# Kernel tuning notes

Hardware: AMD Instinct MI355X
Metric: run time of the kernel (lower is better)

The kernel has to match this reference:

```python
import jax, jax.numpy as jnp
import numpy as np

B, S, D_IN = 4, 2048, 1024
H, D_HEAD = 16, 64  # per-head output dim d_output=64


def setup_inputs() -> dict:
    key = jax.random.key(0)
    ks = jax.random.split(key, 9)
    s_in = 1.0 / np.sqrt(D_IN)
    s_o = 1.0 / np.sqrt(H * D_HEAD)
    return {
        "x": jax.random.normal(ks[0], (B, S, D_IN), dtype=jnp.float32),
        "Wq": jax.random.uniform(ks[1], (H, D_IN, D_HEAD), jnp.float32, -s_in, s_in),
        "bq": jax.random.uniform(ks[2], (H, D_HEAD), jnp.float32, -s_in, s_in),
        "Wk": jax.random.uniform(ks[3], (H, D_IN, D_HEAD), jnp.float32, -s_in, s_in),
        "bk": jax.random.uniform(ks[4], (H, D_HEAD), jnp.float32, -s_in, s_in),
        "Wv": jax.random.uniform(ks[5], (H, D_IN, D_HEAD), jnp.float32, -s_in, s_in),
        "bv": jax.random.uniform(ks[6], (H, D_HEAD), jnp.float32, -s_in, s_in),
        "Wo": jax.random.uniform(ks[7], (H * D_HEAD, D_HEAD), jnp.float32, -s_o, s_o),
        "bo": jax.random.uniform(ks[8], (D_HEAD,), jnp.float32, -s_o, s_o),
    }


def reference(x, Wq, bq, Wk, bk, Wv, bv, Wo, bo):
    # per-head projections: [B,H,S,Dh]
    q = jnp.einsum("bsd,hde->bhse", x, Wq) + bq[None, :, None, :]
    k = jnp.einsum("bsd,hde->bhse", x, Wk) + bk[None, :, None, :]
    v = jnp.einsum("bsd,hde->bhse", x, Wv) + bv[None, :, None, :]
    scale = 1.0 / np.sqrt(D_HEAD)
    scores = jnp.einsum("bhqe,bhke->bhqk", q, k) * scale  # [B,H,S,S]
    seq_len = x.shape[1]
    causal = jnp.tril(jnp.ones((seq_len, seq_len), dtype=bool))
    scores = jnp.where(causal[None, None], scores, -jnp.inf)
    attn = jax.nn.softmax(scores, axis=-1)  # dropout=0 -> identity
    out = jnp.einsum("bhqk,bhke->bhqe", attn, v)  # [B,H,S,Dh]
    # concat heads along feature dim (head order matches torch cat)
    out = out.transpose(0, 2, 1, 3).reshape(x.shape[0], seq_len, H * D_HEAD)
    return out @ Wo + bo
```

## Files before the change

kernel.cpp:

```cpp
#include <hip/hip_runtime.h>

typedef unsigned short u16;
typedef unsigned int u32;
typedef __attribute__((ext_vector_type(8))) short s16x8;
typedef __attribute__((ext_vector_type(4))) float f32x4;

#define MFMA(a,b,c) __builtin_amdgcn_mfma_f32_16x16x32_bf16((a),(b),(c),0,0,0)
#define QSCALE 0.18033688011112042f

__device__ __forceinline__ u16 bfc(float f){
  union { float f; unsigned int u; } c; c.f = f;
  return (u16)((c.u + 0x7fffu + ((c.u >> 16) & 1u)) >> 16);
}
__device__ __forceinline__ u32 pkbf(float lo, float hi){
  union { float f; u32 u; } a, b; a.f = lo; b.f = hi;
  return __builtin_amdgcn_perm(b.u + 0x8000u, a.u + 0x8000u, 0x07060302u);
}
__device__ __forceinline__ float fexp2(float x){ return __builtin_amdgcn_exp2f(x); }
__device__ __forceinline__ f32x4 zero4(){ f32x4 z; z[0]=0.f; z[1]=0.f; z[2]=0.f; z[3]=0.f; return z; }

__device__ __forceinline__ void gload_lds16(const u16* g, u16* l){
  __builtin_amdgcn_global_load_lds((const __attribute__((address_space(1))) unsigned int*)g,
                                   (__attribute__((address_space(3))) unsigned int*)l, 16, 0, 0);
}

__global__ __launch_bounds__(256) void k_cvt(const float* __restrict__ x, u16* __restrict__ xb){
  int i = (blockIdx.x * 256 + threadIdx.x) * 4;
  float4 v = *(const float4*)(x + i);
  *(uint2*)(xb + i) = make_uint2(pkbf(v.x, v.y), pkbf(v.z, v.w));
}

__global__ __launch_bounds__(256) void k_twp(const float* __restrict__ Wq, const float* __restrict__ Wk,
    const float* __restrict__ Wv, const float* __restrict__ Wo,
    u16* __restrict__ wt, u16* __restrict__ wot){
  __shared__ float t[64][65];
  int y = blockIdx.y, k0 = blockIdx.x * 64, tid = threadIdx.x;
  const float* src; u16* dst;
  if (y < 16)      { src = Wq + (size_t)y * 65536;        dst = wt + (size_t)y * 65536; }
  else if (y < 32) { src = Wk + (size_t)(y-16) * 65536;   dst = wt + (size_t)y * 65536; }
  else if (y < 48) { src = Wv + (size_t)(y-32) * 65536;   dst = wt + (size_t)y * 65536; }
  else             { src = Wo;                            dst = wot; }
  const float* s = src + (size_t)k0 * 64;
  int kl = tid >> 2, nc = (tid & 3) * 16;
  #pragma unroll
  for (int j = 0; j < 4; j++){
    float4 v = *(const float4*)(s + kl * 64 + nc + j * 4);
    t[kl][nc + j*4 + 0] = v.x; t[kl][nc + j*4 + 1] = v.y;
    t[kl][nc + j*4 + 2] = v.z; t[kl][nc + j*4 + 3] = v.w;
  }
  __syncthreads();
  int n = tid >> 2, kc = (tid & 3) * 16;
  u16 o[16];
  #pragma unroll
  for (int j = 0; j < 16; j++) o[j] = bfc(t[kc + j][n]);
  u16* d = dst + (size_t)n * 1024 + k0 + kc;
  *(uint4*)(d)     = *(uint4*)&o[0];
  *(uint4*)(d + 8) = *(uint4*)&o[8];
}

__global__ __launch_bounds__(256) void k_qkv(const u16* __restrict__ xb, const u16* __restrict__ wt,
    const float* __restrict__ bq, const float* __restrict__ bk, const float* __restrict__ bv,
    u16* __restrict__ Qo, u16* __restrict__ Ko, u16* __restrict__ VT){
  __shared__ u16 As[128][64];
  __shared__ u16 Bs[128][64];
  int tid = threadIdx.x, wave = tid >> 6, lane = tid & 63;
  int l16 = lane & 15, g = lane >> 4;
  int row0 = blockIdx.x * 128, col0 = blockIdx.y * 128;
  int wm = (wave & 1) * 64, wn = (wave >> 1) * 64;
  f32x4 acc[4][4];
  #pragma unroll
  for (int mt = 0; mt < 4; mt++)
    #pragma unroll
    for (int nt = 0; nt < 4; nt++) acc[mt][nt] = zero4();
  int srow = (lane >> 3);
  int scol = ((lane & 7) ^ srow) * 8;
  for (int k0 = 0; k0 < 1024; k0 += 64){
    __syncthreads();
    #pragma unroll
    for (int p = 0; p < 4; p++){
      int r = wave * 32 + p * 8 + srow;
      gload_lds16(xb + (size_t)(row0 + r) * 1024 + k0 + scol, &As[wave * 32 + p * 8][0]);
      gload_lds16(wt + (size_t)(col0 + r) * 1024 + k0 + scol, &Bs[wave * 32 + p * 8][0]);
    }
    __syncthreads();
    #pragma unroll
    for (int c = 0; c < 2; c++){
      s16x8 af[4], bf[4];
      #pragma unroll
      for (int mt = 0; mt < 4; mt++)
        af[mt] = *(const s16x8*)&As[wm + mt*16 + l16][((c*4 + g) ^ (l16 & 7)) * 8];
      #pragma unroll
      for (int nt = 0; nt < 4; nt++)
        bf[nt] = *(const s16x8*)&Bs[wn + nt*16 + l16][((c*4 + g) ^ (l16 & 7)) * 8];
      #pragma unroll
      for (int mt = 0; mt < 4; mt++)
        #pragma unroll
        for (int nt = 0; nt < 4; nt++) acc[mt][nt] = MFMA(af[mt], bf[nt], acc[mt][nt]);
    }
  }
  #pragma unroll
  for (int nt = 0; nt < 4; nt++){
    int n = col0 + wn + nt * 16 + l16;
    int wi = n >> 10, hh = (n >> 6) & 15, dh = n & 63;
    const float* bptr = (wi == 0) ? bq : (wi == 1) ? bk : bv;
    float bval = bptr[hh * 64 + dh];
    #pragma unroll
    for (int mt = 0; mt < 4; mt++){
      int m0 = row0 + wm + mt * 16 + g * 4;
      int bb = m0 >> 11, ss = m0 & 2047;
      if (wi == 2){
        u32 p0 = pkbf(acc[mt][nt][0] + bval, acc[mt][nt][1] + bval);
        u32 p1 = pkbf(acc[mt][nt][2] + bval, acc[mt][nt][3] + bval);
        *(uint2*)&VT[(((size_t)bb * 16 + hh) * 64 + dh) * 2048 + ss] = make_uint2(p0, p1);
      } else {
        u16* dst = (wi == 0) ? Qo : Ko;
        float scl = (wi == 0) ? QSCALE : 1.0f;
        #pragma unroll
        for (int i = 0; i < 4; i++)
          dst[(((size_t)bb * 16 + hh) * 2048 + ss + i) * 64 + dh] = bfc((acc[mt][nt][i] + bval) * scl);
      }
    }
  }
}

__global__ __launch_bounds__(256, 3) void k_attn(const u16* __restrict__ Q, const u16* __restrict__ Kg,
    const u16* __restrict__ VT, u16* __restrict__ O){
  __shared__ u16 smem[18432];
  u16* Ks = smem;
  u16* Vt = smem + 4608;
  u16* Ps = smem + 9216;
  int hbi = blockIdx.x;
  int qt = 15 - (int)blockIdx.y;
  int b = hbi >> 4, h = hbi & 15;
  int tid = threadIdx.x, wave = tid >> 6, lane = tid & 63;
  int l16 = lane & 15, g = lane >> 4;
  size_t hb = (size_t)hbi * 2048 * 64;
  const u16* kbase = Kg + hb;
  const u16* vbase = VT + hb;
  int sr = tid >> 3, scc = (tid & 7) * 8;
  u16* PsW = Ps + wave * (32 * 72);
  int q0 = qt * 128 + wave * 32;
  s16x8 bq[2][2];
  #pragma unroll
  for (int j = 0; j < 2; j++)
    #pragma unroll
    for (int c = 0; c < 2; c++)
      bq[j][c] = *(const s16x8*)(Q + hb + (size_t)(q0 + j*16 + l16) * 64 + c*32 + g*8);
  f32x4 accO[4][2];
  #pragma unroll
  for (int mt = 0; mt < 4; mt++)
    #pragma unroll
    for (int j = 0; j < 2; j++) accO[mt][j] = zero4();
  float rs0 = 0.f, rs1 = 0.f;
  int nkt = 2 * qt + 2;
  uint4 ka0, ka1, va0, va1;
  ka0 = *(const uint4*)(kbase + (size_t)(sr)      * 64 + scc);
  ka1 = *(const uint4*)(kbase + (size_t)(sr + 32) * 64 + scc);
  va0 = *(const uint4*)(vbase + (size_t)(sr)      * 2048 + scc);
  va1 = *(const uint4*)(vbase + (size_t)(sr + 32) * 2048 + scc);
  *(uint4*)&Ks[sr * 72 + scc] = ka0; *(uint4*)&Ks[(sr + 32) * 72 + scc] = ka1;
  *(uint4*)&Vt[sr * 72 + scc] = va0; *(uint4*)&Vt[(sr + 32) * 72 + scc] = va1;
  __syncthreads();
  for (int kt = 0; kt < nkt; kt++){
    if (kt + 1 < nkt){
      int kb2 = (kt + 1) * 64;
      ka0 = *(const uint4*)(kbase + (size_t)(kb2 + sr)      * 64 + scc);
      ka1 = *(const uint4*)(kbase + (size_t)(kb2 + sr + 32) * 64 + scc);
      va0 = *(const uint4*)(vbase + (size_t)(sr)      * 2048 + kb2 + scc);
      va1 = *(const uint4*)(vbase + (size_t)(sr + 32) * 2048 + kb2 + scc);
    }
    int ks0 = kt * 64;
    if (ks0 <= q0 + 31){
      #pragma unroll
      for (int kb = 0; kb < 4; kb++){
        s16x8 ak0 = *(const s16x8*)&Ks[(kb*16 + l16) * 72 + g*8];
        s16x8 ak1 = *(const s16x8*)&Ks[(kb*16 + l16) * 72 + 32 + g*8];
        #pragma unroll
        for (int j = 0; j < 2; j++){
          f32x4 s = zero4();
          s = MFMA(ak0, bq[j][0], s);
          s = MFMA(ak1, bq[j][1], s);
          if (ks0 + kb*16 + 15 > q0 + j*16){
            int qrow = q0 + j*16 + l16;
            #pragma unroll
            for (int r = 0; r < 4; r++)
              if (ks0 + kb*16 + g*4 + r > qrow) s[r] = -1e30f;
          }
          float p0 = fexp2(s[0]), p1 = fexp2(s[1]), p2 = fexp2(s[2]), p3 = fexp2(s[3]);
          if (j == 0) rs0 += (p0 + p1) + (p2 + p3);
          else        rs1 += (p0 + p1) + (p2 + p3);
          *(uint2*)&PsW[(j*16 + l16) * 72 + kb*16 + g*4] = make_uint2(pkbf(p0, p1), pkbf(p2, p3));
        }
      }
      s16x8 av[4][2];
      #pragma unroll
      for (int mt = 0; mt < 4; mt++)
        #pragma unroll
        for (int kc = 0; kc < 2; kc++)
          av[mt][kc] = *(const s16x8*)&Vt[(mt*16 + l16) * 72 + kc*32 + g*8];
      #pragma unroll
      for (int j = 0; j < 2; j++){
        s16x8 bp0 = *(const s16x8*)&PsW[(j*16 + l16) * 72 + g*8];
        s16x8 bp1 = *(const s16x8*)&PsW[(j*16 + l16) * 72 + 32 + g*8];
        #pragma unroll
        for (int mt = 0; mt < 4; mt++){
          accO[mt][j] = MFMA(av[mt][0], bp0, accO[mt][j]);
          accO[mt][j] = MFMA(av[mt][1], bp1, accO[mt][j]);
        }
      }
    }
    if (kt + 1 < nkt){
      __syncthreads();
      *(uint4*)&Ks[sr * 72 + scc] = ka0; *(uint4*)&Ks[(sr + 32) * 72 + scc] = ka1;
      *(uint4*)&Vt[sr * 72 + scc] = va0; *(uint4*)&Vt[(sr + 32) * 72 + scc] = va1;
      __syncthreads();
    }
  }
  float rinv[2];
  #pragma unroll
  for (int j = 0; j < 2; j++){
    float l = (j == 0) ? rs0 : rs1;
    l += __shfl_xor(l, 16);
    l += __shfl_xor(l, 32);
    rinv[j] = 1.0f / l;
  }
  #pragma unroll
  for (int mt = 0; mt < 4; mt++)
    #pragma unroll
    for (int j = 0; j < 2; j++){
      float o0 = accO[mt][j][0] * rinv[j];
      float o1 = accO[mt][j][1] * rinv[j];
      float o2 = accO[mt][j][2] * rinv[j];
      float o3 = accO[mt][j][3] * rinv[j];
      *(uint2*)&O[((size_t)b * 2048 + q0 + j*16 + l16) * 1024 + h*64 + mt*16 + g*4] =
          make_uint2(pkbf(o0, o1), pkbf(o2, o3));
    }
}

__global__ __launch_bounds__(256) void k_oproj(const u16* __restrict__ Ob, const u16* __restrict__ wot,
    const float* __restrict__ bo, float* __restrict__ out){
  __shared__ u16 As[64][72];
  __shared__ u16 Bs[64][72];
  int rb = blockIdx.x, kc = blockIdx.y;
  int tid = threadIdx.x, wave = tid >> 6, lane = tid & 63;
  int l16 = lane & 15, g = lane >> 4;
  int wr = (wave & 1) * 32, wc = (wave >> 1) * 32;
  int row0 = rb * 64;
  f32x4 acc[2][2];
  acc[0][0]=zero4(); acc[0][1]=zero4(); acc[1][0]=zero4(); acc[1][1]=zero4();
  int r0s = tid >> 3, cc0 = (tid & 7) * 8, r1s = r0s + 32;
  for (int k0 = kc * 256; k0 < kc * 256 + 256; k0 += 64){
    __syncthreads();
    *(uint4*)&As[r0s][cc0] = *(const uint4*)(Ob + (size_t)(row0 + r0s) * 1024 + k0 + cc0);
    *(uint4*)&As[r1s][cc0] = *(const uint4*)(Ob + (size_t)(row0 + r1s) * 1024 + k0 + cc0);
    *(uint4*)&Bs[r0s][cc0] = *(const uint4*)(wot + (size_t)r0s * 1024 + k0 + cc0);
    *(uint4*)&Bs[r1s][cc0] = *(const uint4*)(wot + (size_t)r1s * 1024 + k0 + cc0);
    __syncthreads();
    #pragma unroll
    for (int c = 0; c < 2; c++){
      int kcc = c * 32;
      s16x8 a0 = *(const s16x8*)&As[wr      + l16][kcc + g * 8];
      s16x8 a1 = *(const s16x8*)&As[wr + 16 + l16][kcc + g * 8];
      s16x8 b0 = *(const s16x8*)&Bs[wc      + l16][kcc + g * 8];
      s16x8 b1 = *(const s16x8*)&Bs[wc + 16 + l16][kcc + g * 8];
      acc[0][0] = MFMA(a0, b0, acc[0][0]);
      acc[0][1] = MFMA(a0, b1, acc[0][1]);
      acc[1][0] = MFMA(a1, b0, acc[1][0]);
      acc[1][1] = MFMA(a1, b1, acc[1][1]);
    }
  }
  #pragma unroll
  for (int rt = 0; rt < 2; rt++){
    #pragma unroll
    for (int ct = 0; ct < 2; ct++){
      int col = wc + ct * 16 + l16;
      float bval = (kc == 0) ? bo[col] : 0.f;
      #pragma unroll
      for (int i = 0; i < 4; i++){
        int row = row0 + wr + rt * 16 + g * 4 + i;
        atomicAdd(&out[(size_t)row * 64 + col], acc[rt][ct][i] + bval);
      }
    }
  }
}

extern "C" void kernel_launch(void* const* d_in, const int* in_sizes, int n_in,
                              void* d_out, int out_size, void* d_ws, size_t ws_size,
                              hipStream_t stream){
  const float* x  = (const float*)d_in[0];
  const float* Wq = (const float*)d_in[1];
  const float* bq = (const float*)d_in[2];
  const float* Wk = (const float*)d_in[3];
  const float* bk = (const float*)d_in[4];
  const float* Wv = (const float*)d_in[5];
  const float* bv = (const float*)d_in[6];
  const float* Wo = (const float*)d_in[7];
  const float* bo = (const float*)d_in[8];

  u16* xb  = (u16*)d_ws;
  u16* wt  = xb  + 8388608;
  u16* wot = wt  + 3145728;
  u16* Qb  = wot + 65536;
  u16* Kb  = Qb  + 8388608;
  u16* VTb = Kb  + 8388608;
  u16* Ob  = xb;
  float* out = (float*)d_out;

  hipMemsetAsync(d_out, 0, (size_t)out_size * sizeof(float), stream);
  k_cvt<<<8192, 256, 0, stream>>>(x, xb);
  k_twp<<<dim3(16, 49), 256, 0, stream>>>(Wq, Wk, Wv, Wo, wt, wot);
  k_qkv<<<dim3(64, 24), 256, 0, stream>>>(xb, wt, bq, bk, bv, Qb, Kb, VTb);
  k_attn<<<dim3(64, 16), 256, 0, stream>>>(Qb, Kb, VTb, Ob);
  k_oproj<<<dim3(128, 4), 256, 0, stream>>>(Ob, wot, bo, out);
}
```

Baseline: 234.1 us.

## Restructure QKV GEMM into 256x256 tiles with a four-stage LDS load pipeline

The QKV projection GEMM moves from 128x128 tiles with 4 waves to 256x256 tiles with 8 waves. Four waves load A and four load B into a 4-slot ring buffer that uses a new swizzled layout, and loads run three stages ahead under explicit vmcnt waits and raw barriers. MFMA sections are wrapped in setprio. The aim is more data reuse per tile and overlap of global-to-LDS loads with MFMA work, at the cost of 128 KB of LDS per block, higher register pressure, and only 384 blocks in the grid.

```diff
diff --git a/kernel.cpp b/kernel.cpp
--- a/kernel.cpp
+++ b/kernel.cpp
@@ -7,6 +7,9 @@
 
 #define MFMA(a,b,c) __builtin_amdgcn_mfma_f32_16x16x32_bf16((a),(b),(c),0,0,0)
 #define QSCALE 0.18033688011112042f
+
+#define BAR() do { asm volatile("" ::: "memory"); __builtin_amdgcn_s_barrier(); asm volatile("" ::: "memory"); } while(0)
+#define WAITV(n) asm volatile("s_waitcnt vmcnt(" #n ")" ::: "memory")
 
 __device__ __forceinline__ u16 bfc(float f){
   union { float f; unsigned int u; } c; c.f = f;
@@ -58,55 +61,92 @@
   *(uint4*)(d + 8) = *(uint4*)&o[8];
 }
 
-__global__ __launch_bounds__(256) void k_qkv(const u16* __restrict__ xb, const u16* __restrict__ wt,
+__global__ __launch_bounds__(512, 2) void k_qkv(const u16* __restrict__ xb, const u16* __restrict__ wt,
     const float* __restrict__ bq, const float* __restrict__ bk, const float* __restrict__ bv,
     u16* __restrict__ Qo, u16* __restrict__ Ko, u16* __restrict__ VT){
-  __shared__ u16 As[128][64];
-  __shared__ u16 Bs[128][64];
-  int tid = threadIdx.x, wave = tid >> 6, lane = tid & 63;
+  __shared__ u16 lds[65536];
+  u16* Ab = lds;
+  u16* Bb = lds + 32768;
+  int tid = threadIdx.x, w = tid >> 6, lane = tid & 63;
   int l16 = lane & 15, g = lane >> 4;
-  int row0 = blockIdx.x * 128, col0 = blockIdx.y * 128;
-  int wm = (wave & 1) * 64, wn = (wave >> 1) * 64;
-  f32x4 acc[4][4];
-  #pragma unroll
-  for (int mt = 0; mt < 4; mt++)
+  int wm = w >> 2, wn = w & 3;
+  int row0 = blockIdx.x * 256, col0 = blockIdx.y * 256;
+  f32x4 acc[8][4];
+  #pragma unroll
+  for (int mt = 0; mt < 8; mt++)
     #pragma unroll
     for (int nt = 0; nt < 4; nt++) acc[mt][nt] = zero4();
-  int srow = (lane >> 3);
-  int scol = ((lane & 7) ^ srow) * 8;
-  for (int k0 = 0; k0 < 1024; k0 += 64){
-    __syncthreads();
-    #pragma unroll
-    for (int p = 0; p < 4; p++){
-      int r = wave * 32 + p * 8 + srow;
-      gload_lds16(xb + (size_t)(row0 + r) * 1024 + k0 + scol, &As[wave * 32 + p * 8][0]);
-      gload_lds16(wt + (size_t)(col0 + r) * 1024 + k0 + scol, &Bs[wave * 32 + p * 8][0]);
-    }
-    __syncthreads();
-    #pragma unroll
-    for (int c = 0; c < 2; c++){
-      s16x8 af[4], bf[4];
-      #pragma unroll
-      for (int mt = 0; mt < 4; mt++)
-        af[mt] = *(const s16x8*)&As[wm + mt*16 + l16][((c*4 + g) ^ (l16 & 7)) * 8];
+
+  bool isB = (w >= 4);
+  int wseg = (w & 3) * 4;
+  const u16* gsrc = isB ? wt : xb;
+  int gbase0 = isB ? col0 : row0;
+  const u16* gp[4];
+  #pragma unroll
+  for (int j = 0; j < 4; j++){
+    int sg = wseg + j;
+    int r = sg * 8 + (lane >> 3);
+    int pc = lane & 7;
+    int lc = pc ^ (r & 7);
+    int m = 2 * r + (lc >> 2);
+    int kk = (lc & 3) * 8;
+    gp[j] = gsrc + (size_t)(gbase0 + m) * 1024 + kk;
+  }
+  u16* lring = isB ? Bb : Ab;
+
+  auto stage = [&](int s3){
+    u16* lslot = lring + (s3 & 3) * 8192;
+    int ko = s3 * 32;
+    #pragma unroll
+    for (int j = 0; j < 4; j++)
+      gload_lds16(gp[j] + ko, lslot + (wseg + j) * 512);
+  };
+
+  auto phase = [&](int s){
+    const u16* Asl = Ab + (s & 3) * 8192;
+    const u16* Bsl = Bb + (s & 3) * 8192;
+    s16x8 af[8], bf[4];
+    #pragma unroll
+    for (int nt = 0; nt < 4; nt++){
+      int nr = wn * 64 + nt * 16 + l16;
+      int r = nr >> 1, pc = (((nr & 1) << 2) | g) ^ (r & 7);
+      bf[nt] = *(const s16x8*)&Bsl[r * 64 + pc * 8];
+    }
+    #pragma unroll
+    for (int mt = 0; mt < 8; mt++){
+      int mr = wm * 128 + mt * 16 + l16;
+      int r = mr >> 1, pc = (((mr & 1) << 2) | g) ^ (r & 7);
+      af[mt] = *(const s16x8*)&Asl[r * 64 + pc * 8];
+    }
+    __builtin_amdgcn_s_setprio(1);
+    #pragma unroll
+    for (int mt = 0; mt < 8; mt++)
       #pragma unroll
       for (int nt = 0; nt < 4; nt++)
-        bf[nt] = *(const s16x8*)&Bs[wn + nt*16 + l16][((c*4 + g) ^ (l16 & 7)) * 8];
-      #pragma unroll
-      for (int mt = 0; mt < 4; mt++)
-        #pragma unroll
-        for (int nt = 0; nt < 4; nt++) acc[mt][nt] = MFMA(af[mt], bf[nt], acc[mt][nt]);
-    }
-  }
+        acc[mt][nt] = MFMA(af[mt], bf[nt], acc[mt][nt]);
+    __builtin_amdgcn_s_setprio(0);
+  };
+
+  stage(0); stage(1); stage(2);
+  for (int s = 0; s < 29; ++s){
+    WAITV(8);
+    BAR();
+    stage(s + 3);
+    phase(s);
+  }
+  WAITV(8); BAR(); phase(29);
+  WAITV(4); BAR(); phase(30);
+  WAITV(0); BAR(); phase(31);
+
   #pragma unroll
   for (int nt = 0; nt < 4; nt++){
-    int n = col0 + wn + nt * 16 + l16;
+    int n = col0 + wn * 64 + nt * 16 + l16;
     int wi = n >> 10, hh = (n >> 6) & 15, dh = n & 63;
     const float* bptr = (wi == 0) ? bq : (wi == 1) ? bk : bv;
     float bval = bptr[hh * 64 + dh];
     #pragma unroll
-    for (int mt = 0; mt < 4; mt++){
-      int m0 = row0 + wm + mt * 16 + g * 4;
+    for (int mt = 0; mt < 8; mt++){
+      int m0 = row0 + wm * 128 + mt * 16 + g * 4;
       int bb = m0 >> 11, ss = m0 & 2047;
       if (wi == 2){
         u32 p0 = pkbf(acc[mt][nt][0] + bval, acc[mt][nt][1] + bval);
@@ -309,7 +349,7 @@
   hipMemsetAsync(d_out, 0, (size_t)out_size * sizeof(float), stream);
   k_cvt<<<8192, 256, 0, stream>>>(x, xb);
   k_twp<<<dim3(16, 49), 256, 0, stream>>>(Wq, Wk, Wv, Wo, wt, wot);
-  k_qkv<<<dim3(64, 24), 256, 0, stream>>>(xb, wt, bq, bk, bv, Qb, Kb, VTb);
+  k_qkv<<<dim3(32, 12), 512, 0, stream>>>(xb, wt, bq, bk, bv, Qb, Kb, VTb);
   k_attn<<<dim3(64, 16), 256, 0, stream>>>(Qb, Kb, VTb, Ob);
   k_oproj<<<dim3(128, 4), 256, 0, stream>>>(Ob, wot, bo, out);
 }
```

Result: slower. 238.8 us (+2.0%).

## Double-buffer QKV projection GEMM K-loop with async LDS prefetch

Applied to the files above, without the earlier changes.

Restructures the QKV projection GEMM main loop to use a 32-wide K step with two LDS buffers. The next tile is prefetched via global_load_lds while MFMAs run on the current one, with one barrier per step instead of two. It adds s_setprio around the MFMA block and a new XOR swizzle for the narrower rows. The trade-off is twice as many loop iterations with less MFMA work per barrier.

```diff
diff --git a/kernel.cpp b/kernel.cpp
--- a/kernel.cpp
+++ b/kernel.cpp
@@ -7,6 +7,9 @@
 
 #define MFMA(a,b,c) __builtin_amdgcn_mfma_f32_16x16x32_bf16((a),(b),(c),0,0,0)
 #define QSCALE 0.18033688011112042f
+
+#define BAR() do { asm volatile("" ::: "memory"); __builtin_amdgcn_s_barrier(); asm volatile("" ::: "memory"); } while(0)
+#define WAITV0() asm volatile("s_waitcnt vmcnt(0)" ::: "memory")
 
 __device__ __forceinline__ u16 bfc(float f){
   union { float f; unsigned int u; } c; c.f = f;
@@ -61,43 +64,69 @@
 __global__ __launch_bounds__(256) void k_qkv(const u16* __restrict__ xb, const u16* __restrict__ wt,
     const float* __restrict__ bq, const float* __restrict__ bk, const float* __restrict__ bv,
     u16* __restrict__ Qo, u16* __restrict__ Ko, u16* __restrict__ VT){
-  __shared__ u16 As[128][64];
-  __shared__ u16 Bs[128][64];
-  int tid = threadIdx.x, wave = tid >> 6, lane = tid & 63;
+  __shared__ u16 lds[16384];
+  int tid = threadIdx.x, w = tid >> 6, lane = tid & 63;
   int l16 = lane & 15, g = lane >> 4;
   int row0 = blockIdx.x * 128, col0 = blockIdx.y * 128;
-  int wm = (wave & 1) * 64, wn = (wave >> 1) * 64;
+  int wm = (w & 1) * 64, wn = (w >> 1) * 64;
   f32x4 acc[4][4];
   #pragma unroll
   for (int mt = 0; mt < 4; mt++)
     #pragma unroll
     for (int nt = 0; nt < 4; nt++) acc[mt][nt] = zero4();
-  int srow = (lane >> 3);
-  int scol = ((lane & 7) ^ srow) * 8;
-  for (int k0 = 0; k0 < 1024; k0 += 64){
-    __syncthreads();
-    #pragma unroll
-    for (int p = 0; p < 4; p++){
-      int r = wave * 32 + p * 8 + srow;
-      gload_lds16(xb + (size_t)(row0 + r) * 1024 + k0 + scol, &As[wave * 32 + p * 8][0]);
-      gload_lds16(wt + (size_t)(col0 + r) * 1024 + k0 + scol, &Bs[wave * 32 + p * 8][0]);
-    }
-    __syncthreads();
-    #pragma unroll
-    for (int c = 0; c < 2; c++){
-      s16x8 af[4], bf[4];
-      #pragma unroll
-      for (int mt = 0; mt < 4; mt++)
-        af[mt] = *(const s16x8*)&As[wm + mt*16 + l16][((c*4 + g) ^ (l16 & 7)) * 8];
-      #pragma unroll
-      for (int nt = 0; nt < 4; nt++)
-        bf[nt] = *(const s16x8*)&Bs[wn + nt*16 + l16][((c*4 + g) ^ (l16 & 7)) * 8];
-      #pragma unroll
-      for (int mt = 0; mt < 4; mt++)
-        #pragma unroll
-        for (int nt = 0; nt < 4; nt++) acc[mt][nt] = MFMA(af[mt], bf[nt], acc[mt][nt]);
-    }
-  }
+
+  int trow = tid >> 2;
+  int lc = (tid & 3) ^ ((tid >> 3) & 3);
+  const u16* gpa = xb + (size_t)(row0 + trow) * 1024 + lc * 8;
+  const u16* gpb = wt + (size_t)(col0 + trow) * 1024 + lc * 8;
+  u16* lA0 = &lds[w * 512];
+  u16* lA1 = &lds[2048 + w * 512];
+  u16* lB0 = &lds[8192 + w * 512];
+  u16* lB1 = &lds[8192 + 2048 + w * 512];
+
+  int afo[4], bfo[4];
+  #pragma unroll
+  for (int mt = 0; mt < 4; mt++){
+    int r = wm + mt * 16 + l16;
+    afo[mt] = r * 32 + ((g ^ ((r >> 1) & 3)) * 8);
+  }
+  #pragma unroll
+  for (int nt = 0; nt < 4; nt++){
+    int r = wn + nt * 16 + l16;
+    bfo[nt] = 8192 + r * 32 + ((g ^ ((r >> 1) & 3)) * 8);
+  }
+
+  gload_lds16(gpa,              lA0);
+  gload_lds16(gpa + 64 * 1024,  lA1);
+  gload_lds16(gpb,              lB0);
+  gload_lds16(gpb + 64 * 1024,  lB1);
+  WAITV0(); BAR();
+
+  #pragma unroll 2
+  for (int s = 0; s < 32; ++s){
+    if (s < 31){
+      int ko = (s + 1) * 32;
+      int dsel = ((s + 1) & 1) * 4096;
+      gload_lds16(gpa + ko,             lA0 + dsel);
+      gload_lds16(gpa + ko + 64 * 1024, lA1 + dsel);
+      gload_lds16(gpb + ko,             lB0 + dsel);
+      gload_lds16(gpb + ko + 64 * 1024, lB1 + dsel);
+    }
+    int sel = (s & 1) * 4096;
+    s16x8 af[4], bf[4];
+    #pragma unroll
+    for (int mt = 0; mt < 4; mt++) af[mt] = *(const s16x8*)&lds[sel + afo[mt]];
+    #pragma unroll
+    for (int nt = 0; nt < 4; nt++) bf[nt] = *(const s16x8*)&lds[sel + bfo[nt]];
+    __builtin_amdgcn_s_setprio(1);
+    #pragma unroll
+    for (int mt = 0; mt < 4; mt++)
+      #pragma unroll
+      for (int nt = 0; nt < 4; nt++) acc[mt][nt] = MFMA(af[mt], bf[nt], acc[mt][nt]);
+    __builtin_amdgcn_s_setprio(0);
+    WAITV0(); BAR();
+  }
+
   #pragma unroll
   for (int nt = 0; nt < 4; nt++){
     int n = col0 + wn + nt * 16 + l16;
```

New measurement: 232.2 us. No clear change (-0.8%).

## Restructure QKV GEMM with 256x128 tiles, 3-stage LDS pipeline and tile swizzle

Applied to the files above, without the earlier changes.

Rewrites the QKV projection GEMM to use 512-thread blocks on 256x128 output tiles with K-steps of 32. Global-to-LDS loads are triple-buffered with explicit vmcnt waits and raw barriers, so copies overlap the MFMA work. The block index is swizzled for L2 locality, and MFMA issue priority is raised while the MFMAs run. This targets load latency and sync stalls in the GEMM, at the cost of more LDS per block and hand-managed waitcnt ordering that can break correctness if the counts are wrong.

```diff
diff --git a/kernel.cpp b/kernel.cpp
--- a/kernel.cpp
+++ b/kernel.cpp
@@ -7,6 +7,9 @@
 
 #define MFMA(a,b,c) __builtin_amdgcn_mfma_f32_16x16x32_bf16((a),(b),(c),0,0,0)
 #define QSCALE 0.18033688011112042f
+
+#define BAR() do { asm volatile("" ::: "memory"); __builtin_amdgcn_s_barrier(); asm volatile("" ::: "memory"); } while(0)
+#define WAITV(n) asm volatile("s_waitcnt vmcnt(" #n ")" ::: "memory")
 
 __device__ __forceinline__ u16 bfc(float f){
   union { float f; unsigned int u; } c; c.f = f;
@@ -58,55 +61,75 @@
   *(uint4*)(d + 8) = *(uint4*)&o[8];
 }
 
-__global__ __launch_bounds__(256) void k_qkv(const u16* __restrict__ xb, const u16* __restrict__ wt,
+__global__ __launch_bounds__(512, 2) void k_qkv(const u16* __restrict__ xb, const u16* __restrict__ wt,
     const float* __restrict__ bq, const float* __restrict__ bk, const float* __restrict__ bv,
     u16* __restrict__ Qo, u16* __restrict__ Ko, u16* __restrict__ VT){
-  __shared__ u16 As[128][64];
-  __shared__ u16 Bs[128][64];
-  int tid = threadIdx.x, wave = tid >> 6, lane = tid & 63;
+  __shared__ u16 lds[36864];
+  int tid = threadIdx.x, w = tid >> 6, lane = tid & 63;
   int l16 = lane & 15, g = lane >> 4;
-  int row0 = blockIdx.x * 128, col0 = blockIdx.y * 128;
-  int wm = (wave & 1) * 64, wn = (wave >> 1) * 64;
+  int lin = (int)blockIdx.y * 32 + (int)blockIdx.x;
+  int swz = (lin & 7) * 96 + (lin >> 3);
+  int row0 = (swz & 31) * 256, col0 = (swz >> 5) * 128;
+  int wm = w >> 1, wn = w & 1;
   f32x4 acc[4][4];
   #pragma unroll
   for (int mt = 0; mt < 4; mt++)
     #pragma unroll
     for (int nt = 0; nt < 4; nt++) acc[mt][nt] = zero4();
-  int srow = (lane >> 3);
-  int scol = ((lane & 7) ^ srow) * 8;
-  for (int k0 = 0; k0 < 1024; k0 += 64){
-    __syncthreads();
-    #pragma unroll
-    for (int p = 0; p < 4; p++){
-      int r = wave * 32 + p * 8 + srow;
-      gload_lds16(xb + (size_t)(row0 + r) * 1024 + k0 + scol, &As[wave * 32 + p * 8][0]);
-      gload_lds16(wt + (size_t)(col0 + r) * 1024 + k0 + scol, &Bs[wave * 32 + p * 8][0]);
-    }
-    __syncthreads();
-    #pragma unroll
-    for (int c = 0; c < 2; c++){
-      s16x8 af[4], bf[4];
-      #pragma unroll
-      for (int mt = 0; mt < 4; mt++)
-        af[mt] = *(const s16x8*)&As[wm + mt*16 + l16][((c*4 + g) ^ (l16 & 7)) * 8];
-      #pragma unroll
-      for (int nt = 0; nt < 4; nt++)
-        bf[nt] = *(const s16x8*)&Bs[wn + nt*16 + l16][((c*4 + g) ^ (l16 & 7)) * 8];
-      #pragma unroll
-      for (int mt = 0; mt < 4; mt++)
-        #pragma unroll
-        for (int nt = 0; nt < 4; nt++) acc[mt][nt] = MFMA(af[mt], bf[nt], acc[mt][nt]);
-    }
+
+  int trow = tid >> 2;
+  int lc = (tid & 3) ^ ((tid >> 3) & 3);
+  const u16* gpa0 = xb + (size_t)(row0 + trow) * 1024 + lc * 8;
+  const u16* gpa1 = xb + (size_t)(row0 + 128 + trow) * 1024 + lc * 8;
+  const u16* gpb  = wt + (size_t)(col0 + trow) * 1024 + lc * 8;
+
+  int afo[4], bfo[4];
+  #pragma unroll
+  for (int mt = 0; mt < 4; mt++){
+    int r = wm * 64 + mt * 16 + l16;
+    afo[mt] = r * 32 + ((g ^ ((r >> 1) & 3)) * 8);
   }
   #pragma unroll
   for (int nt = 0; nt < 4; nt++){
-    int n = col0 + wn + nt * 16 + l16;
+    int r = wn * 64 + nt * 16 + l16;
+    bfo[nt] = 8192 + r * 32 + ((g ^ ((r >> 1) & 3)) * 8);
+  }
+
+#define STAGE(T2, SB) do { int ko_ = (T2) * 32; \
+    gload_lds16(gpa0 + ko_, &lds[(SB) + w * 512]); \
+    gload_lds16(gpa1 + ko_, &lds[(SB) + 4096 + w * 512]); \
+    gload_lds16(gpb  + ko_, &lds[(SB) + 8192 + w * 512]); } while(0)
+
+#define COMPUTE(SB) do { s16x8 af[4], bf[4]; \
+    _Pragma("unroll") for (int mt = 0; mt < 4; mt++) af[mt] = *(const s16x8*)&lds[(SB) + afo[mt]]; \
+    _Pragma("unroll") for (int nt = 0; nt < 4; nt++) bf[nt] = *(const s16x8*)&lds[(SB) + bfo[nt]]; \
+    __builtin_amdgcn_s_setprio(1); \
+    _Pragma("unroll") for (int mt = 0; mt < 4; mt++) \
+      _Pragma("unroll") for (int nt = 0; nt < 4; nt++) acc[mt][nt] = MFMA(af[mt], bf[nt], acc[mt][nt]); \
+    __builtin_amdgcn_s_setprio(0); } while(0)
+
+  STAGE(0, 0); STAGE(1, 12288);
+  WAITV(3); BAR();
+  for (int t = 0; t < 30; t += 3){
+    STAGE(t + 2, 24576); COMPUTE(0);     WAITV(3); BAR();
+    STAGE(t + 3, 0);     COMPUTE(12288); WAITV(3); BAR();
+    STAGE(t + 4, 12288); COMPUTE(24576); WAITV(3); BAR();
+  }
+  COMPUTE(0);
+  WAITV(0); BAR();
+  COMPUTE(12288);
+#undef STAGE
+#undef COMPUTE
+
+  #pragma unroll
+  for (int nt = 0; nt < 4; nt++){
+    int n = col0 + wn * 64 + nt * 16 + l16;
     int wi = n >> 10, hh = (n >> 6) & 15, dh = n & 63;
     const float* bptr = (wi == 0) ? bq : (wi == 1) ? bk : bv;
     float bval = bptr[hh * 64 + dh];
     #pragma unroll
     for (int mt = 0; mt < 4; mt++){
-      int m0 = row0 + wm + mt * 16 + g * 4;
+      int m0 = row0 + wm * 64 + mt * 16 + g * 4;
       int bb = m0 >> 11, ss = m0 & 2047;
       if (wi == 2){
         u32 p0 = pkbf(acc[mt][nt][0] + bval, acc[mt][nt][1] + bval);
@@ -309,7 +332,7 @@
   hipMemsetAsync(d_out, 0, (size_t)out_size * sizeof(float), stream);
   k_cvt<<<8192, 256, 0, stream>>>(x, xb);
   k_twp<<<dim3(16, 49), 256, 0, stream>>>(Wq, Wk, Wv, Wo, wt, wot);
-  k_qkv<<<dim3(64, 24), 256, 0, stream>>>(xb, wt, bq, bk, bv, Qb, Kb, VTb);
+  k_qkv<<<dim3(32, 24), 512, 0, stream>>>(xb, wt, bq, bk, bv, Qb, Kb, VTb);
   k_attn<<<dim3(64, 16), 256, 0, stream>>>(Qb, Kb, VTb, Ob);
   k_oproj<<<dim3(128, 4), 256, 0, stream>>>(Ob, wot, bo, out);
 }
```

Result: slower. 247.5 us (+5.7%).
